# Kernel optimization log

Measured on AMD Instinct MI355X. Metric: run time of the kernel, lower is better.

Reference implementation:

```python
import jax, jax.numpy as jnp
import numpy as np
from jax import lax

B, T, E, H, L, V = 32, 1024, 256, 512, 3, 10000
EPS = 1e-3  # Keras BatchNormalization default epsilon


def setup_inputs() -> dict:
    key = jax.random.key(0)
    ks = jax.random.split(key, 12)
    s = 0.05
    x = jax.random.randint(ks[0], (B, T), 0, V)
    emb = jax.random.normal(ks[1], (V, E), jnp.float32) * s
    k0 = jax.random.normal(ks[2], (E, 3 * H), jnp.float32) * s
    rk0 = jax.random.normal(ks[3], (H, 3 * H), jnp.float32) * s
    b0 = jax.random.normal(ks[4], (2, 3 * H), jnp.float32) * s
    krest = jax.random.normal(ks[5], (L - 1, H, 3 * H), jnp.float32) * s
    rkrest = jax.random.normal(ks[6], (L - 1, H, 3 * H), jnp.float32) * s
    brest = jax.random.normal(ks[7], (L - 1, 2, 3 * H), jnp.float32) * s
    gammas = jnp.ones((L, H), jnp.float32)
    betas = jnp.zeros((L, H), jnp.float32)
    return {"x": x, "emb": emb, "k0": k0, "rk0": rk0, "b0": b0,
            "krest": krest, "rkrest": rkrest, "brest": brest,
            "gammas": gammas, "betas": betas}


def _gru_layer(x_seq, h0, kernel, rkernel, bias):
    # Keras GRU, reset_after=True, activation=relu, recurrent_activation=sigmoid
    bi, br = bias[0], bias[1]
    xproj = jnp.einsum('bte,eh->bth', x_seq, kernel) + bi  # [B,T,3H]

    def step(h, xp):
        inner = h @ rkernel + br
        xz, xr, xh = jnp.split(xp, 3, axis=-1)
        hz, hr, hh = jnp.split(inner, 3, axis=-1)
        z = jax.nn.sigmoid(xz + hz)
        r = jax.nn.sigmoid(xr + hr)
        cand = jax.nn.relu(xh + r * hh)
        h_new = z * h + (1.0 - z) * cand
        return h_new, h_new

    hT, ys = lax.scan(step, h0, jnp.swapaxes(xproj, 0, 1))  # scan over T
    return jnp.swapaxes(ys, 0, 1), hT  # [B,T,H], [B,H]


def _batchnorm(y, gamma, beta):
    # training-mode BN over (batch, time), channel axis last
    mean = jnp.mean(y, axis=(0, 1))
    var = jnp.var(y, axis=(0, 1))
    return gamma * (y - mean) * lax.rsqrt(var + EPS) + beta


def reference(x, emb, k0, rk0, b0, krest, rkrest, brest, gammas, betas):
    h = jnp.zeros((B, H), jnp.float32)  # stateful GRU after reset_states()
    y = emb[x]  # [B,T,E] embedding lookup
    y, state = _gru_layer(y, h, k0, rk0, b0)
    y = _batchnorm(y, gammas[0], betas[0])
    for i in range(L - 1):  # subsequent layers get previous layer's state
        y, state = _gru_layer(y, state, krest[i], rkrest[i], brest[i])
        y = _batchnorm(y, gammas[i + 1], betas[i + 1])
    return y, state
```

## Files before the change

kernel.cpp:

```cpp
#include <hip/hip_runtime.h>
#include <hip/hip_bf16.h>

#define BB 32
#define TT 1024
#define EE 256
#define HH 512
#define H3 1536
#define MM (BB*TT)
#define NWG 16
#define EPS_BN 1e-3f

typedef __attribute__((ext_vector_type(8))) short bf16x8;
typedef __attribute__((ext_vector_type(4))) float f32x4;

__device__ __forceinline__ unsigned short f2bf(float f){
  unsigned u = __float_as_uint(f);
  u += 0x7fffu + ((u>>16)&1u);
  return (unsigned short)(u>>16);
}
__device__ __forceinline__ float bf2f(unsigned short u){
  return __uint_as_float(((unsigned)u)<<16);
}
__device__ __forceinline__ uint4 ld16_coh(const void* p){
  uint4 r;
  asm volatile("global_load_dwordx4 %0, %1, off sc0 sc1" : "=v"(r) : "v"(p) : "memory");
  return r;
}
__device__ __forceinline__ void st8_coh(void* p, uint2 v){
  asm volatile("global_store_dwordx2 %0, %1, off sc0 sc1" :: "v"(p), "v"(v) : "memory");
}

__global__ __launch_bounds__(256) void conv_transpose(
    const float* __restrict__ in, unsigned short* __restrict__ out, int K, int N){
  __shared__ float tile[32][33];
  int k0 = blockIdx.x*32, n0 = blockIdx.y*32;
  int tx = threadIdx.x & 31, ty = threadIdx.x >> 5;
  for(int i=ty;i<32;i+=8) tile[i][tx] = in[(size_t)(k0+i)*N + n0 + tx];
  __syncthreads();
  for(int i=ty;i<32;i+=8) out[(size_t)(n0+i)*K + k0 + tx] = f2bf(tile[tx][i]);
}

__global__ __launch_bounds__(256) void gather_emb(
    const int* __restrict__ x, const float* __restrict__ emb,
    unsigned short* __restrict__ y0){
  int i = blockIdx.x*256 + threadIdx.x;
  if(i >= MM*EE/4) return;
  int row = i >> 6;
  int c4 = (i & 63) << 2;
  int t = row >> 5, b = row & 31;
  float4 v = *(const float4*)&emb[(size_t)x[b*TT + t]*EE + c4];
  ushort4 o; o.x=f2bf(v.x); o.y=f2bf(v.y); o.z=f2bf(v.z); o.w=f2bf(v.w);
  *(ushort4*)&y0[(size_t)row*EE + c4] = o;
}

__global__ __launch_bounds__(256) void gemm_bias(
    const unsigned short* __restrict__ A,
    const unsigned short* __restrict__ BT,
    const float* __restrict__ bias,
    float* __restrict__ C, int Mdim, int Ndim, int Kdim){
  __shared__ __align__(16) unsigned short sA[64][72];
  __shared__ __align__(16) unsigned short sB[64][72];
  int m0 = blockIdx.x*64, n0 = blockIdx.y*64;
  int tid = threadIdx.x, ln = tid & 63, wv = tid >> 6;
  int wm = wv >> 1, wn = wv & 1;
  f32x4 acc[2][2] = {};
  for(int k0=0;k0<Kdim;k0+=64){
    __syncthreads();
    for(int p2=0;p2<2;p2++){
      int idx = (p2*256 + tid)*8;
      int r = idx >> 6, c = idx & 63;
      *(uint4*)&sA[r][c] = *(const uint4*)&A[(size_t)(m0+r)*Kdim + k0 + c];
      *(uint4*)&sB[r][c] = *(const uint4*)&BT[(size_t)(n0+r)*Kdim + k0 + c];
    }
    __syncthreads();
    for(int kk=0;kk<64;kk+=32){
      int kf = kk + ((ln>>4)<<3);
      bf16x8 af[2], bfr[2];
      for(int i=0;i<2;i++){
        af[i]  = *(const bf16x8*)&sA[wm*32 + i*16 + (ln&15)][kf];
        bfr[i] = *(const bf16x8*)&sB[wn*32 + i*16 + (ln&15)][kf];
      }
      for(int mi=0;mi<2;mi++)
        for(int ni=0;ni<2;ni++)
          acc[mi][ni] = __builtin_amdgcn_mfma_f32_16x16x32_bf16(af[mi], bfr[ni], acc[mi][ni], 0,0,0);
    }
  }
  for(int mi=0;mi<2;mi++)
    for(int ni=0;ni<2;ni++){
      int gn = n0 + wn*32 + ni*16 + (ln&15);
      float bs = bias ? bias[gn] : 0.f;
      int gm0 = m0 + wm*32 + mi*16 + ((ln>>4)<<2);
      for(int r2=0;r2<4;r2++)
        C[(size_t)(gm0+r2)*Ndim + gn] = acc[mi][ni][r2] + bs;
    }
}

__global__ __launch_bounds__(256,1) void gru_scan(
    const float* __restrict__ xproj,
    const unsigned short* __restrict__ rkT,
    const float* __restrict__ br,
    float* __restrict__ hstate,
    unsigned short* __restrict__ ybf,
    float* __restrict__ stats,
    unsigned short* Hbuf,
    int* flags, int C, int wbase){
  __shared__ __align__(16) unsigned short hlds[32][520];
  __shared__ float sredA[4][16];
  __shared__ float sredQ[4][16];
  const int wg = blockIdx.x, c0 = wg*32;
  const int tid = threadIdx.x, ln = tid & 63, wv = tid >> 6;
  const int wch = wv >> 1, wb = wv & 1;
  const int q = ln >> 4;
  const int frow = ln & 15;
  const int b = wb*16 + frow;
  const int chb = c0 + wch*16 + (q<<2);
  const int kofs = q << 3;

  bf16x8 wf[3][16];
  #pragma unroll
  for(int g=0; g<3; g++){
    const unsigned short* wsrc = &rkT[(size_t)(g*HH + c0 + wch*16 + frow)*HH];
    #pragma unroll
    for(int kk=0; kk<16; kk++)
      wf[g][kk] = *(const bf16x8*)&wsrc[kk*32 + kofs];
  }
  const f32x4 brz4 = *(const f32x4*)&br[0*HH + chb];
  const f32x4 brr4 = *(const f32x4*)&br[1*HH + chb];
  const f32x4 brh4 = *(const f32x4*)&br[2*HH + chb];

  f32x4 hv = *(const f32x4*)&hstate[b*HH + chb];
  {
    uint2 o;
    o.x = ((unsigned)f2bf(hv[1])<<16) | f2bf(hv[0]);
    o.y = ((unsigned)f2bf(hv[3])<<16) | f2bf(hv[2]);
    st8_coh(&Hbuf[(size_t)b*HH + chb], o);
  }
  asm volatile("s_waitcnt vmcnt(0)" ::: "memory");
  __syncthreads();
  if(tid==0) __hip_atomic_store(&flags[wg*16], wbase+1, __ATOMIC_RELAXED, __HIP_MEMORY_SCOPE_AGENT);
  f32x4 as = {0,0,0,0}, aq = {0,0,0,0};

  for(int s=0; s<C; s++){
    const int par = s & 1;
    const float* xp = &xproj[(size_t)s*BB*H3 + (size_t)b*H3];
    f32x4 xz4 = *(const f32x4*)&xp[chb];
    f32x4 xr4 = *(const f32x4*)&xp[HH + chb];
    f32x4 xh4 = *(const f32x4*)&xp[2*HH + chb];
    if(wv==0){
      const int need = wbase + s + 1;
      int guard = 0; bool done = false;
      while(!done && guard < 5000){
        int v = (ln < NWG) ? __hip_atomic_load(&flags[ln*16], __ATOMIC_RELAXED, __HIP_MEMORY_SCOPE_AGENT)
                           : 0x7fffffff;
        done = __all(v >= need) != 0;
        guard++;
      }
    }
    __syncthreads();
    {
      const unsigned short* src = &Hbuf[(size_t)par*BB*HH];
      uint4 hb[8];
      #pragma unroll
      for(int j=0;j<8;j++) hb[j] = ld16_coh(&src[(j*256 + tid)*8]);
      asm volatile("s_waitcnt vmcnt(0)" ::: "memory");
      #pragma unroll
      for(int j=0;j<8;j++){
        int i = (j*256 + tid)*8;
        *(uint4*)&hlds[i>>9][i&511] = hb[j];
      }
    }
    __syncthreads();
    f32x4 acc[3] = {};
    #pragma unroll
    for(int kk=0; kk<16; kk++){
      bf16x8 hf = *(const bf16x8*)&hlds[b][kk*32 + kofs];
      acc[0] = __builtin_amdgcn_mfma_f32_16x16x32_bf16(wf[0][kk], hf, acc[0], 0,0,0);
      acc[1] = __builtin_amdgcn_mfma_f32_16x16x32_bf16(wf[1][kk], hf, acc[1], 0,0,0);
      acc[2] = __builtin_amdgcn_mfma_f32_16x16x32_bf16(wf[2][kk], hf, acc[2], 0,0,0);
    }
    #pragma unroll
    for(int r2=0;r2<4;r2++){
      float z  = 1.f/(1.f + __expf(-(xz4[r2] + acc[0][r2] + brz4[r2])));
      float rr = 1.f/(1.f + __expf(-(xr4[r2] + acc[1][r2] + brr4[r2])));
      float cd = fmaxf(xh4[r2] + rr*(acc[2][r2] + brh4[r2]), 0.f);
      float hn = z*hv[r2] + (1.f - z)*cd;
      hv[r2] = hn;
      as[r2] += hn; aq[r2] += hn*hn;
    }
    uint2 o;
    o.x = ((unsigned)f2bf(hv[1])<<16) | f2bf(hv[0]);
    o.y = ((unsigned)f2bf(hv[3])<<16) | f2bf(hv[2]);
    st8_coh(&Hbuf[((size_t)(1-par)*BB + b)*HH + chb], o);
    asm volatile("s_waitcnt vmcnt(0)" ::: "memory");
    __syncthreads();
    if(tid==0) __hip_atomic_store(&flags[wg*16], wbase+s+2, __ATOMIC_RELAXED, __HIP_MEMORY_SCOPE_AGENT);
    *(uint2*)&ybf[((size_t)s*BB + b)*HH + chb] = o;
  }
  *(f32x4*)&hstate[b*HH + chb] = hv;
  #pragma unroll
  for(int d=1; d<16; d<<=1){
    #pragma unroll
    for(int r2=0;r2<4;r2++){
      as[r2] += __shfl_xor(as[r2], d);
      aq[r2] += __shfl_xor(aq[r2], d);
    }
  }
  if(frow==0){
    #pragma unroll
    for(int r2=0;r2<4;r2++){
      sredA[wv][(q<<2)+r2] = as[r2];
      sredQ[wv][(q<<2)+r2] = aq[r2];
    }
  }
  __syncthreads();
  if(tid < 32){
    int i = tid & 15, wc = tid >> 4;
    stats[c0 + wc*16 + i]      += sredA[wc*2][i] + sredA[wc*2+1][i];
    stats[HH + c0 + wc*16 + i] += sredQ[wc*2][i] + sredQ[wc*2+1][i];
  }
}

__global__ void bn_prep(const float* __restrict__ stats,
                        const float* __restrict__ gamma, const float* __restrict__ beta,
                        float* __restrict__ scsh){
  int c = blockIdx.x*256 + threadIdx.x;
  if(c >= HH) return;
  const float inv = 1.f/(float)MM;
  float mean = stats[c]*inv;
  float var  = stats[HH+c]*inv - mean*mean;
  float s = gamma[c]*rsqrtf(var + EPS_BN);
  scsh[c] = s; scsh[HH+c] = beta[c] - mean*s;
}

__global__ __launch_bounds__(256) void kscale(
    const unsigned short* __restrict__ kT, const float* __restrict__ scsh,
    const float* __restrict__ bias, unsigned short* __restrict__ kTs,
    float* __restrict__ badj){
  int n = blockIdx.x*4 + (threadIdx.x >> 6);
  int ln = threadIdx.x & 63;
  int k = ln*8;
  uint4 v = *(const uint4*)&kT[(size_t)n*HH + k];
  unsigned short* pv = (unsigned short*)&v;
  unsigned short ov[8];
  float acc = 0.f;
  for(int j=0;j<8;j++){
    float f = bf2f(pv[j]);
    acc += scsh[HH + k + j] * f;
    ov[j] = f2bf(f * scsh[k + j]);
  }
  *(uint4*)&kTs[(size_t)n*HH + k] = *(uint4*)ov;
  for(int d=1; d<64; d<<=1) acc += __shfl_xor(acc, d);
  if(ln==0) badj[n] = bias[n] + acc;
}

__global__ __launch_bounds__(256) void final_out(
    const unsigned short* __restrict__ ybf, const float* __restrict__ scsh,
    float* __restrict__ out){
  int row = blockIdx.x*4 + (threadIdx.x >> 6);
  int ln = threadIdx.x & 63;
  int t = row >> 5, b = row & 31;
  int k = ln*8;
  uint4 v = *(const uint4*)&ybf[(size_t)row*HH + k];
  unsigned short* pv = (unsigned short*)&v;
  float o[8];
  for(int j=0;j<8;j++) o[j] = bf2f(pv[j])*scsh[k+j] + scsh[HH+k+j];
  float4* dst = (float4*)&out[((size_t)b*TT + t)*HH + k];
  dst[0] = make_float4(o[0],o[1],o[2],o[3]);
  dst[1] = make_float4(o[4],o[5],o[6],o[7]);
}

__global__ void copy_f32(const float* __restrict__ in, float* __restrict__ out, int n){
  int i = blockIdx.x*blockDim.x + threadIdx.x;
  if(i<n) out[i] = in[i];
}

extern "C" void kernel_launch(void* const* d_in, const int* in_sizes, int n_in,
                              void* d_out, int out_size, void* d_ws, size_t ws_size,
                              hipStream_t stream){
  const int*   x      = (const int*)d_in[0];
  const float* emb    = (const float*)d_in[1];
  const float* k0     = (const float*)d_in[2];
  const float* rk0    = (const float*)d_in[3];
  const float* b0     = (const float*)d_in[4];
  const float* krest  = (const float*)d_in[5];
  const float* rkrest = (const float*)d_in[6];
  const float* brest  = (const float*)d_in[7];
  const float* gammas = (const float*)d_in[8];
  const float* betas  = (const float*)d_in[9];
  float* out_y = (float*)d_out;
  float* out_state = out_y + (size_t)MM*HH;

  char* p = (char*)d_ws;
  auto alloc = [&](size_t bytes)->void*{ void* r = p; p += (bytes + 255) & ~(size_t)255; return r; };
  unsigned short* ybf  = (unsigned short*)alloc((size_t)MM*HH*2);
  unsigned short* y0bf = (unsigned short*)alloc((size_t)MM*EE*2);
  unsigned short* kT0  = (unsigned short*)alloc((size_t)H3*EE*2);
  unsigned short* kT1  = (unsigned short*)alloc((size_t)H3*HH*2);
  unsigned short* kT2  = (unsigned short*)alloc((size_t)H3*HH*2);
  unsigned short* rkT0 = (unsigned short*)alloc((size_t)H3*HH*2);
  unsigned short* rkT1 = (unsigned short*)alloc((size_t)H3*HH*2);
  unsigned short* rkT2 = (unsigned short*)alloc((size_t)H3*HH*2);
  unsigned short* kTs  = (unsigned short*)alloc((size_t)H3*HH*2);
  float* badj   = (float*)alloc(H3*4);
  float* scsh   = (float*)alloc(2*HH*4);
  float* stats  = (float*)alloc(2*HH*4);
  float* hstate = (float*)alloc((size_t)BB*HH*4);
  unsigned short* Hbuf = (unsigned short*)alloc((size_t)2*BB*HH*2);
  int* flags = (int*)alloc(NWG*16*4);
  size_t fixed_bytes = (size_t)(p - (char*)d_ws);

  int C = 64;
  const int cands[4] = {1024, 512, 256, 128};
  for(int i=0;i<4;i++){
    if(fixed_bytes + (size_t)cands[i]*BB*H3*4 <= ws_size){ C = cands[i]; break; }
  }
  float* xproj = (float*)alloc((size_t)C*BB*H3*4);
  const int NC = TT / C;

  hipMemsetAsync(flags, 0, NWG*16*4, stream);
  hipMemsetAsync(hstate, 0, (size_t)BB*HH*4, stream);

  conv_transpose<<<dim3(EE/32, H3/32), 256, 0, stream>>>(k0, kT0, EE, H3);
  conv_transpose<<<dim3(HH/32, H3/32), 256, 0, stream>>>(krest, kT1, HH, H3);
  conv_transpose<<<dim3(HH/32, H3/32), 256, 0, stream>>>(krest + (size_t)HH*H3, kT2, HH, H3);
  conv_transpose<<<dim3(HH/32, H3/32), 256, 0, stream>>>(rk0, rkT0, HH, H3);
  conv_transpose<<<dim3(HH/32, H3/32), 256, 0, stream>>>(rkrest, rkT1, HH, H3);
  conv_transpose<<<dim3(HH/32, H3/32), 256, 0, stream>>>(rkrest + (size_t)HH*H3, rkT2, HH, H3);
  gather_emb<<<(MM*EE/4 + 255)/256, 256, 0, stream>>>(x, emb, y0bf);

  for(int L=0; L<3; L++){
    hipMemsetAsync(stats, 0, 2*HH*4, stream);
    const unsigned short* A; const unsigned short* BT; const float* bias;
    const unsigned short* rk; const float* rbias; int Kd;
    if(L == 0){
      A = y0bf; BT = kT0; bias = b0; rk = rkT0; rbias = b0 + H3; Kd = EE;
    } else {
      const unsigned short* kTn = (L==1) ? kT1 : kT2;
      const float* bn_bias = (L==1) ? brest : brest + 2*H3;
      kscale<<<H3/4, 256, 0, stream>>>(kTn, scsh, bn_bias, kTs, badj);
      A = ybf; BT = kTs; bias = badj; Kd = HH;
      rk = (L==1) ? rkT1 : rkT2;
      rbias = (L==1) ? brest + H3 : brest + 3*H3;
    }
    for(int c=0;c<NC;c++){
      int t0 = c*C;
      gemm_bias<<<dim3(C*BB/64, H3/64), 256, 0, stream>>>(
          A + (size_t)t0*BB*Kd, BT, bias, xproj, C*BB, H3, Kd);
      gru_scan<<<NWG, 256, 0, stream>>>(
          xproj, rk, rbias, hstate, ybf + (size_t)t0*BB*HH,
          stats, Hbuf, flags, C, L*(TT+1) + t0);
    }
    bn_prep<<<2, 256, 0, stream>>>(stats, gammas + L*HH, betas + L*HH, scsh);
  }
  final_out<<<MM/4, 256, 0, stream>>>(ybf, scsh, out_y);
  copy_f32<<<64, 256, 0, stream>>>(hstate, out_state, BB*HH);
}
```

Measured before the change: 10.22 ms.

## Split GRU scan workgroups by batch half to decouple synchronization groups

The recurrent scan is repartitioned so each of the 16 workgroups owns 64 hidden channels for one half of the batch (16 rows), instead of 32 channels for all 32 rows. Each workgroup now waits only on the 8 peers sharing its batch half and loads only half of the hidden state into LDS per step, which reduces global traffic and the cross-workgroup barrier fan-in. BatchNorm statistics are kept in two per-half buffers and summed in bn_prep. The spin-wait guard is also raised.

```diff
diff --git a/kernel.cpp b/kernel.cpp
--- a/kernel.cpp
+++ b/kernel.cpp
@@ -104,22 +104,23 @@
     float* __restrict__ stats,
     unsigned short* Hbuf,
     int* flags, int C, int wbase){
-  __shared__ __align__(16) unsigned short hlds[32][520];
+  __shared__ __align__(16) unsigned short hlds[16][520];
   __shared__ float sredA[4][16];
   __shared__ float sredQ[4][16];
-  const int wg = blockIdx.x, c0 = wg*32;
+  const int wg = blockIdx.x;
+  const int cg = wg >> 1, bg = wg & 1;
+  const int chbase = cg*64;
   const int tid = threadIdx.x, ln = tid & 63, wv = tid >> 6;
-  const int wch = wv >> 1, wb = wv & 1;
-  const int q = ln >> 4;
-  const int frow = ln & 15;
-  const int b = wb*16 + frow;
-  const int chb = c0 + wch*16 + (q<<2);
+  const int q = ln >> 4, frow = ln & 15;
+  const int b = bg*16 + frow;
+  const int chb = chbase + wv*16 + (q<<2);
+  const int wrow = chbase + wv*16 + frow;
   const int kofs = q << 3;
 
   bf16x8 wf[3][16];
   #pragma unroll
   for(int g=0; g<3; g++){
-    const unsigned short* wsrc = &rkT[(size_t)(g*HH + c0 + wch*16 + frow)*HH];
+    const unsigned short* wsrc = &rkT[(size_t)(g*HH + wrow)*HH];
     #pragma unroll
     for(int kk=0; kk<16; kk++)
       wf[g][kk] = *(const bf16x8*)&wsrc[kk*32 + kofs];
@@ -149,22 +150,22 @@
     if(wv==0){
       const int need = wbase + s + 1;
       int guard = 0; bool done = false;
-      while(!done && guard < 5000){
-        int v = (ln < NWG) ? __hip_atomic_load(&flags[ln*16], __ATOMIC_RELAXED, __HIP_MEMORY_SCOPE_AGENT)
-                           : 0x7fffffff;
+      while(!done && guard < 200000){
+        int v = (ln < 8) ? __hip_atomic_load(&flags[(ln*2+bg)*16], __ATOMIC_RELAXED, __HIP_MEMORY_SCOPE_AGENT)
+                         : 0x7fffffff;
         done = __all(v >= need) != 0;
         guard++;
       }
     }
     __syncthreads();
     {
-      const unsigned short* src = &Hbuf[(size_t)par*BB*HH];
-      uint4 hb[8];
+      const unsigned short* src = &Hbuf[(size_t)par*BB*HH + (size_t)bg*16*HH];
+      uint4 hb[4];
       #pragma unroll
-      for(int j=0;j<8;j++) hb[j] = ld16_coh(&src[(j*256 + tid)*8]);
+      for(int j=0;j<4;j++) hb[j] = ld16_coh(&src[(j*256 + tid)*8]);
       asm volatile("s_waitcnt vmcnt(0)" ::: "memory");
       #pragma unroll
-      for(int j=0;j<8;j++){
+      for(int j=0;j<4;j++){
         int i = (j*256 + tid)*8;
         *(uint4*)&hlds[i>>9][i&511] = hb[j];
       }
@@ -173,7 +174,7 @@
     f32x4 acc[3] = {};
     #pragma unroll
     for(int kk=0; kk<16; kk++){
-      bf16x8 hf = *(const bf16x8*)&hlds[b][kk*32 + kofs];
+      bf16x8 hf = *(const bf16x8*)&hlds[frow][kk*32 + kofs];
       acc[0] = __builtin_amdgcn_mfma_f32_16x16x32_bf16(wf[0][kk], hf, acc[0], 0,0,0);
       acc[1] = __builtin_amdgcn_mfma_f32_16x16x32_bf16(wf[1][kk], hf, acc[1], 0,0,0);
       acc[2] = __builtin_amdgcn_mfma_f32_16x16x32_bf16(wf[2][kk], hf, acc[2], 0,0,0);
@@ -213,10 +214,10 @@
     }
   }
   __syncthreads();
-  if(tid < 32){
-    int i = tid & 15, wc = tid >> 4;
-    stats[c0 + wc*16 + i]      += sredA[wc*2][i] + sredA[wc*2+1][i];
-    stats[HH + c0 + wc*16 + i] += sredQ[wc*2][i] + sredQ[wc*2+1][i];
+  if(tid < 64){
+    float* st = stats + (size_t)bg*2*HH;
+    st[chbase + tid]      += sredA[tid>>4][tid&15];
+    st[HH + chbase + tid] += sredQ[tid>>4][tid&15];
   }
 }
 
@@ -226,8 +227,10 @@
   int c = blockIdx.x*256 + threadIdx.x;
   if(c >= HH) return;
   const float inv = 1.f/(float)MM;
-  float mean = stats[c]*inv;
-  float var  = stats[HH+c]*inv - mean*mean;
+  float s0 = stats[c] + stats[2*HH + c];
+  float q0 = stats[HH + c] + stats[3*HH + c];
+  float mean = s0*inv;
+  float var  = q0*inv - mean*mean;
   float s = gamma[c]*rsqrtf(var + EPS_BN);
   scsh[c] = s; scsh[HH+c] = beta[c] - mean*s;
 }
@@ -303,7 +306,7 @@
   unsigned short* kTs  = (unsigned short*)alloc((size_t)H3*HH*2);
   float* badj   = (float*)alloc(H3*4);
   float* scsh   = (float*)alloc(2*HH*4);
-  float* stats  = (float*)alloc(2*HH*4);
+  float* stats  = (float*)alloc(2*2*HH*4);
   float* hstate = (float*)alloc((size_t)BB*HH*4);
   unsigned short* Hbuf = (unsigned short*)alloc((size_t)2*BB*HH*2);
   int* flags = (int*)alloc(NWG*16*4);
@@ -329,7 +332,7 @@
   gather_emb<<<(MM*EE/4 + 255)/256, 256, 0, stream>>>(x, emb, y0bf);
 
   for(int L=0; L<3; L++){
-    hipMemsetAsync(stats, 0, 2*HH*4, stream);
+    hipMemsetAsync(stats, 0, 2*2*HH*4, stream);
     const unsigned short* A; const unsigned short* BT; const float* bias;
     const unsigned short* rk; const float* rbias; int Kd;
     if(L == 0){
```

Result: faster. 9.126 ms (-10.7%).
